# Kernel optimization log

Measured on AMD Instinct MI355X. Metric: run time of the kernel, lower is better.

The kernel has to match this reference:

```python
import jax, jax.numpy as jnp
import numpy as np

S, B, K = 64, 16, 512
QD, KD, A = 512, 512, 256


def setup_inputs() -> dict:
    key = jax.random.key(0)
    ks = jax.random.split(key, 10)
    inv_q = 1.0 / np.sqrt(QD)
    inv_k = 1.0 / np.sqrt(KD)
    inv_a = 1.0 / np.sqrt(A)
    return {
        "queries": jax.random.normal(ks[0], (S, B, QD), dtype=jnp.float32),
        "keys": jax.random.normal(ks[1], (B, K, KD), dtype=jnp.float32),
        "null_mask": jax.random.randint(ks[2], (B, K), 0, 2).astype(jnp.bool_),
        # nn.Linear params (PyTorch layout: weight (out, in), bias (out,))
        "Ww": jax.random.uniform(ks[3], (A, QD), jnp.float32, -inv_q, inv_q),
        "Wb": jax.random.uniform(ks[4], (A,), jnp.float32, -inv_q, inv_q),
        "Uw": jax.random.uniform(ks[5], (A, KD), jnp.float32, -inv_k, inv_k),
        "Ub": jax.random.uniform(ks[6], (A,), jnp.float32, -inv_k, inv_k),
        "vw": jax.random.uniform(ks[7], (1, A), jnp.float32, -inv_a, inv_a),
        "vb": jax.random.uniform(ks[8], (1,), jnp.float32, -inv_a, inv_a),
    }


def reference(queries, keys, null_mask, Ww, Wb, Uw, Ub, vw, vb):
    # t_query: (S, B, A); t_key: (B, K, A)
    t_query = jnp.einsum("sbq,aq->sba", queries, Ww) + Wb
    t_key = jnp.einsum("bkd,ad->bka", keys, Uw) + Ub
    # broadcast add -> (S, B, K, A), tanh, project with v -> alpha (S, B, K)
    h = jnp.tanh(t_query[:, :, None, :] + t_key[None, :, :, :])
    alpha = jnp.einsum("sbka,a->sbk", h, vw[0]) + vb[0]
    alpha = jnp.where(null_mask[None, :, :], -jnp.inf, alpha)
    att_weight = jax.nn.softmax(alpha, axis=2)  # (S, B, K)
    # bmm(att_weight^T, keys)^T -> (S, B, KD)
    attened_keys = jnp.einsum("sbk,bkd->sbd", att_weight, keys)
    return attened_keys, alpha
```

## Files before the change

kernel.cpp:

```cpp
#include <hip/hip_runtime.h>
#include <math.h>

#define S_DIM 64
#define B_DIM 16
#define K_DIM 512
#define QD_DIM 512
#define A_DIM 256

#define NEG_BIG (-3.0e38f)

#define SC 2.8853900817779268f

#define TK_OFF 262144
#define W_WS_OFF ((size_t)2359296)
#define PART_OFF ((size_t)2883584)
#define CONV_F32_OFF ((size_t)4980736)
#define CONV_ROWS 9728
#define LO_USHORT_OFF ((size_t)CONV_ROWS * 512)

typedef __attribute__((ext_vector_type(8))) short short8v;
typedef __attribute__((ext_vector_type(4))) float f32x4;

static __device__ __forceinline__ uint2 pack_hi4(float4 v) {
    unsigned x0 = __float_as_uint(v.x), x1 = __float_as_uint(v.y),
             x2 = __float_as_uint(v.z), x3 = __float_as_uint(v.w);
    uint2 r;
    r.x = (x1 & 0xffff0000u) | (x0 >> 16);
    r.y = (x3 & 0xffff0000u) | (x2 >> 16);
    return r;
}
static __device__ __forceinline__ uint2 pack_lo4(float4 v) {
    float l0 = v.x - __uint_as_float(__float_as_uint(v.x) & 0xffff0000u);
    float l1 = v.y - __uint_as_float(__float_as_uint(v.y) & 0xffff0000u);
    float l2 = v.z - __uint_as_float(__float_as_uint(v.z) & 0xffff0000u);
    float l3 = v.w - __uint_as_float(__float_as_uint(v.w) & 0xffff0000u);
    unsigned y0 = __float_as_uint(l0), y1 = __float_as_uint(l1),
             y2 = __float_as_uint(l2), y3 = __float_as_uint(l3);
    uint2 r;
    r.x = (y1 & 0xffff0000u) | (y0 >> 16);
    r.y = (y3 & 0xffff0000u) | (y2 >> 16);
    return r;
}

__global__ __launch_bounds__(256) void conv_kernel(
    const float* __restrict__ q, const float* __restrict__ k,
    const float* __restrict__ ww, const float* __restrict__ uw,
    unsigned short* __restrict__ hi, unsigned short* __restrict__ lo)
{
    const int idx = blockIdx.x * 256 + threadIdx.x;
    const int row = idx >> 6;
    const int c   = (idx & 63) << 3;

    const float* __restrict__ src;
    if (row < 1024)      src = q  + (size_t)row * 512;
    else if (row < 9216) src = k  + (size_t)(row - 1024) * 512;
    else if (row < 9472) src = ww + (size_t)(row - 9216) * 512;
    else                 src = uw + (size_t)(row - 9472) * 512;

    float4 v0 = *(const float4*)(src + c);
    float4 v1 = *(const float4*)(src + c + 4);
    uint2 h0 = pack_hi4(v0), h1 = pack_hi4(v1);
    uint2 l0 = pack_lo4(v0), l1 = pack_lo4(v1);
    uint4 H = {h0.x, h0.y, h1.x, h1.y};
    uint4 L = {l0.x, l0.y, l1.x, l1.y};
    *(uint4*)&hi[(size_t)row * 512 + c] = H;
    *(uint4*)&lo[(size_t)row * 512 + c] = L;
}

__global__ __launch_bounds__(256) void lin_mfma(
    const unsigned short* __restrict__ hi, const unsigned short* __restrict__ lo,
    const float* __restrict__ Wb, const float* __restrict__ Ub,
    float* __restrict__ t_ws)
{
    __shared__ unsigned short Ah[64][40], Al[64][40], Bh[64][40], Bl[64][40];

    const int bx = blockIdx.x;
    const bool isQ = (bx < 64);
    int mt, nt;
    if (isQ) { mt = bx >> 2; nt = bx & 3; }
    else     { int t = bx - 64; mt = t >> 7; nt = t & 127; }

    const int aro = isQ ? (mt * 64) : (9472 + mt * 64);
    const int bro = isQ ? (9216 + nt * 64) : (1024 + nt * 64);

    const int tid  = threadIdx.x;
    const int srow = tid >> 2;
    const int scol = (tid & 3) << 3;
    const int lane = tid & 63, wid = tid >> 6;
    const int wm = (wid >> 1) << 5, wn = (wid & 1) << 5;
    const int fr  = lane & 15;
    const int fkb = (lane >> 4) << 3;

    f32x4 acc[2][2] = {};

    const unsigned short* pAh = hi + (size_t)(aro + srow) * 512 + scol;
    const unsigned short* pAl = lo + (size_t)(aro + srow) * 512 + scol;
    const unsigned short* pBh = hi + (size_t)(bro + srow) * 512 + scol;
    const unsigned short* pBl = lo + (size_t)(bro + srow) * 512 + scol;

    uint4 c_ah = *(const uint4*)(pAh);
    uint4 c_al = *(const uint4*)(pAl);
    uint4 c_bh = *(const uint4*)(pBh);
    uint4 c_bl = *(const uint4*)(pBl);
    uint4 n_ah = *(const uint4*)(pAh + 32);
    uint4 n_al = *(const uint4*)(pAl + 32);
    uint4 n_bh = *(const uint4*)(pBh + 32);
    uint4 n_bl = *(const uint4*)(pBl + 32);

    for (int ks = 0; ks < 16; ++ks) {
        __syncthreads();
        *(uint4*)&Ah[srow][scol] = c_ah;
        *(uint4*)&Al[srow][scol] = c_al;
        *(uint4*)&Bh[srow][scol] = c_bh;
        *(uint4*)&Bl[srow][scol] = c_bl;
        __syncthreads();
        c_ah = n_ah; c_al = n_al; c_bh = n_bh; c_bl = n_bl;
        if (ks < 14) {
            const int o = (ks + 2) * 32;
            n_ah = *(const uint4*)(pAh + o);
            n_al = *(const uint4*)(pAl + o);
            n_bh = *(const uint4*)(pBh + o);
            n_bl = *(const uint4*)(pBl + o);
        }
        short8v bhv[2], blv[2];
        #pragma unroll
        for (int j = 0; j < 2; ++j) {
            bhv[j] = *(const short8v*)&Bh[wn + j * 16 + fr][fkb];
            blv[j] = *(const short8v*)&Bl[wn + j * 16 + fr][fkb];
        }
        #pragma unroll
        for (int i = 0; i < 2; ++i) {
            short8v ah = *(const short8v*)&Ah[wm + i * 16 + fr][fkb];
            short8v al = *(const short8v*)&Al[wm + i * 16 + fr][fkb];
            #pragma unroll
            for (int j = 0; j < 2; ++j) {
                acc[i][j] = __builtin_amdgcn_mfma_f32_16x16x32_bf16(ah, bhv[j], acc[i][j], 0, 0, 0);
                acc[i][j] = __builtin_amdgcn_mfma_f32_16x16x32_bf16(ah, blv[j], acc[i][j], 0, 0, 0);
                acc[i][j] = __builtin_amdgcn_mfma_f32_16x16x32_bf16(al, bhv[j], acc[i][j], 0, 0, 0);
            }
        }
    }

    const int crow = (lane >> 4) << 2;
    if (isQ) {
        #pragma unroll
        for (int j = 0; j < 2; ++j) {
            const int a_col = nt * 64 + wn + j * 16 + fr;
            const float bias = Wb[a_col];
            #pragma unroll
            for (int i = 0; i < 2; ++i)
                #pragma unroll
                for (int r = 0; r < 4; ++r) {
                    const int m = mt * 64 + wm + i * 16 + crow + r;
                    t_ws[(size_t)m * 256 + a_col] =
                        __builtin_amdgcn_exp2f(SC * (acc[i][j][r] + bias));
                }
        }
    } else {
        #pragma unroll
        for (int i = 0; i < 2; ++i)
            #pragma unroll
            for (int r = 0; r < 4; ++r) {
                const int a = mt * 64 + wm + i * 16 + crow + r;
                const float bias = Ub[a];
                #pragma unroll
                for (int j = 0; j < 2; ++j) {
                    const int n = nt * 64 + wn + j * 16 + fr;
                    t_ws[TK_OFF + (size_t)(n >> 9) * 131072 + (size_t)a * 512 + (n & 511)]
                        = __builtin_amdgcn_exp2f(SC * (acc[i][j][r] + bias));
                }
            }
    }
}

__global__ __launch_bounds__(256) void alpha_part_kernel(
    const float* __restrict__ t_ws, const float* __restrict__ vw,
    float* __restrict__ part)
{
    __shared__ float4 pv[64];

    const int bid = blockIdx.x;
    const int b     = bid >> 7;
    const int inner = bid & 127;
    const int ah    = inner >> 5;
    const int sp    = (inner & 31) << 1;
    const int a0    = ah << 6;
    const int tid = threadIdx.x;

    if (tid < 64) {
        const int a = a0 + tid;
        float4 p;
        p.x = t_ws[(size_t)(sp * B_DIM + b) * A_DIM + a];
        p.y = t_ws[(size_t)((sp + 1) * B_DIM + b) * A_DIM + a];
        p.z = vw[a]; p.w = 0.f;
        pv[tid] = p;
    }
    __syncthreads();

    const float* __restrict__ ek =
        t_ws + TK_OFF + (size_t)b * 131072 + (size_t)a0 * 512;
    const int k2 = tid * 2;

    float acc00 = 0.f, acc01 = 0.f, acc10 = 0.f, acc11 = 0.f;
    #pragma unroll 4
    for (int a = 0; a < 64; ++a) {
        float2 tv = *(const float2*)&ek[(size_t)a * 512 + k2];
        float4 p = pv[a];
        float r00 = __builtin_amdgcn_rcpf(fmaf(p.x, tv.x, 1.0f));
        float r01 = __builtin_amdgcn_rcpf(fmaf(p.x, tv.y, 1.0f));
        float r10 = __builtin_amdgcn_rcpf(fmaf(p.y, tv.x, 1.0f));
        float r11 = __builtin_amdgcn_rcpf(fmaf(p.y, tv.y, 1.0f));
        acc00 = fmaf(p.z, r00, acc00);
        acc01 = fmaf(p.z, r01, acc01);
        acc10 = fmaf(p.z, r10, acc10);
        acc11 = fmaf(p.z, r11, acc11);
    }

    const int sb0 = sp * B_DIM + b;
    float* __restrict__ pp = part + (size_t)ah * 524288;
    *(float2*)&pp[(size_t)sb0 * 512 + k2]           = make_float2(acc00, acc01);
    *(float2*)&pp[(size_t)(sb0 + B_DIM) * 512 + k2] = make_float2(acc10, acc11);
}

__global__ __launch_bounds__(256) void softmax_kernel(
    const float* __restrict__ part, const float* __restrict__ vw,
    const float* __restrict__ vb, const unsigned char* __restrict__ mask,
    float* __restrict__ alpha_out, float* __restrict__ w_ws)
{
    __shared__ float red[3][4];

    const int bid = blockIdx.x;
    const int s = bid >> 4, b = bid & 15;
    const int sb = s * B_DIM + b;
    const int tid = threadIdx.x;
    const int lane = tid & 63, wid = tid >> 6;

    float sv = vw[tid];
    #pragma unroll
    for (int o = 32; o > 0; o >>= 1) sv += __shfl_xor(sv, o);
    if (lane == 0) red[0][wid] = sv;
    __syncthreads();
    const float base = red[0][0] + red[0][1] + red[0][2] + red[0][3] + vb[0];

    const int k2 = tid * 2;
    const size_t po = (size_t)sb * 512 + k2;
    float2 p0 = *(const float2*)&part[po];
    float2 p1 = *(const float2*)&part[po + 524288];
    float2 p2 = *(const float2*)&part[po + 2 * 524288];
    float2 p3 = *(const float2*)&part[po + 3 * 524288];
    float a0 = base - 2.0f * (p0.x + p1.x + p2.x + p3.x);
    float a1 = base - 2.0f * (p0.y + p1.y + p2.y + p3.y);

    const unsigned char* mrow = mask + b * K_DIM;
    if (mrow[k2])     a0 = NEG_BIG;
    if (mrow[k2 + 1]) a1 = NEG_BIG;

    *(float2*)&alpha_out[(size_t)sb * K_DIM + k2] = make_float2(a0, a1);

    float m = fmaxf(a0, a1);
    #pragma unroll
    for (int o = 32; o > 0; o >>= 1) m = fmaxf(m, __shfl_xor(m, o));
    if (lane == 0) red[1][wid] = m;
    __syncthreads();
    const float mx = fmaxf(fmaxf(red[1][0], red[1][1]), fmaxf(red[1][2], red[1][3]));

    float e0 = __expf(a0 - mx);
    float e1 = __expf(a1 - mx);
    float ssum = e0 + e1;
    #pragma unroll
    for (int o = 32; o > 0; o >>= 1) ssum += __shfl_xor(ssum, o);
    if (lane == 0) red[2][wid] = ssum;
    __syncthreads();
    const float inv = 1.0f / (red[2][0] + red[2][1] + red[2][2] + red[2][3]);

    *(float2*)&w_ws[(size_t)(b * S_DIM + s) * K_DIM + k2] = make_float2(e0 * inv, e1 * inv);
}

__global__ __launch_bounds__(256) void att_kernel(
    const float* __restrict__ w_ws, const float* __restrict__ keys,
    float* __restrict__ out_att)
{
    __shared__ float wt[16][68];
    __shared__ float kt[64][64];

    const int d0g = blockIdx.x * 64;
    const int s0  = blockIdx.y * 16;
    const int b   = blockIdx.z;
    const int tid = threadIdx.x;

    const int sL = tid >> 4;
    const int dc = (tid & 15) << 2;

    float acc[4] = {};

    for (int k0 = 0; k0 < K_DIM; k0 += 64) {
        __syncthreads();
        *(float4*)&wt[sL][dc] =
            *(const float4*)&w_ws[(size_t)(b * S_DIM + s0 + sL) * K_DIM + k0 + dc];
        #pragma unroll
        for (int rr = 0; rr < 4; ++rr) {
            const int kr = (tid >> 4) + rr * 16;
            *(float4*)&kt[kr][dc] =
                *(const float4*)&keys[((size_t)b * K_DIM + k0 + kr) * QD_DIM + d0g + dc];
        }
        __syncthreads();
        #pragma unroll
        for (int kk = 0; kk < 64; kk += 4) {
            float4 wv = *(const float4*)&wt[sL][kk];
            float wr[4] = {wv.x, wv.y, wv.z, wv.w};
            #pragma unroll
            for (int u = 0; u < 4; ++u) {
                float4 kv = *(const float4*)&kt[kk + u][dc];
                acc[0] = fmaf(wr[u], kv.x, acc[0]);
                acc[1] = fmaf(wr[u], kv.y, acc[1]);
                acc[2] = fmaf(wr[u], kv.z, acc[2]);
                acc[3] = fmaf(wr[u], kv.w, acc[3]);
            }
        }
    }

    float4 o = {acc[0], acc[1], acc[2], acc[3]};
    *(float4*)&out_att[(size_t)((s0 + sL) * B_DIM + b) * QD_DIM + d0g + dc] = o;
}

extern "C" void kernel_launch(void* const* d_in, const int* in_sizes, int n_in,
                              void* d_out, int out_size, void* d_ws, size_t ws_size,
                              hipStream_t stream) {
    const float* queries = (const float*)d_in[0];
    const float* keys    = (const float*)d_in[1];
    const unsigned char* mask = (const unsigned char*)d_in[2];
    const float* Ww = (const float*)d_in[3];
    const float* Wb = (const float*)d_in[4];
    const float* Uw = (const float*)d_in[5];
    const float* Ub = (const float*)d_in[6];
    const float* vw = (const float*)d_in[7];
    const float* vb = (const float*)d_in[8];

    float* out_att   = (float*)d_out;
    float* out_alpha = (float*)d_out + (size_t)S_DIM * B_DIM * QD_DIM;

    float* t_ws = (float*)d_ws;
    float* w_ws = t_ws + W_WS_OFF;
    float* part = t_ws + PART_OFF;
    unsigned short* hi = (unsigned short*)(t_ws + CONV_F32_OFF);
    unsigned short* lo = hi + LO_USHORT_OFF;

    conv_kernel<<<2432, 256, 0, stream>>>(queries, keys, Ww, Uw, hi, lo);

    lin_mfma<<<576, 256, 0, stream>>>(hi, lo, Wb, Ub, t_ws);

    alpha_part_kernel<<<2048, 256, 0, stream>>>(t_ws, vw, part);

    softmax_kernel<<<1024, 256, 0, stream>>>(part, vw, vb, mask,
                                             out_alpha, w_ws);

    dim3 gC(QD_DIM / 64, S_DIM / 16, B_DIM);
    att_kernel<<<gC, 256, 0, stream>>>(w_ws, keys, out_att);
}
```

Before: 143.4 us.

## Fuse alpha partial-sum kernel into softmax kernel, dropping partials buffer

Merges the alpha partial-sum kernel (split over four A chunks and two s rows per block) with the softmax kernel, so each block computes the full 256-wide A reduction for one (s,b) row and then does masking and softmax in place. This removes one launch and the write and read of a 2M-float partials buffer. In exchange each block now loops over all of A serially with only one s row per block, losing the reuse of t_key loads across two s rows and reducing parallelism per output element. Block order is remapped so that pairs of b alternate, which appears aimed at L2 locality of t_key across blocks.

```diff
diff --git a/kernel.cpp b/kernel.cpp
--- a/kernel.cpp
+++ b/kernel.cpp
@@ -13,8 +13,7 @@
 
 #define TK_OFF 262144
 #define W_WS_OFF ((size_t)2359296)
-#define PART_OFF ((size_t)2883584)
-#define CONV_F32_OFF ((size_t)4980736)
+#define CONV_F32_OFF ((size_t)2883584)
 #define CONV_ROWS 9728
 #define LO_USHORT_OFF ((size_t)CONV_ROWS * 512)
 
@@ -173,84 +172,54 @@
     }
 }
 
-__global__ __launch_bounds__(256) void alpha_part_kernel(
+__global__ __launch_bounds__(256) void alpha_kernel(
     const float* __restrict__ t_ws, const float* __restrict__ vw,
-    float* __restrict__ part)
-{
-    __shared__ float4 pv[64];
-
-    const int bid = blockIdx.x;
-    const int b     = bid >> 7;
-    const int inner = bid & 127;
-    const int ah    = inner >> 5;
-    const int sp    = (inner & 31) << 1;
-    const int a0    = ah << 6;
-    const int tid = threadIdx.x;
-
-    if (tid < 64) {
-        const int a = a0 + tid;
-        float4 p;
-        p.x = t_ws[(size_t)(sp * B_DIM + b) * A_DIM + a];
-        p.y = t_ws[(size_t)((sp + 1) * B_DIM + b) * A_DIM + a];
-        p.z = vw[a]; p.w = 0.f;
-        pv[tid] = p;
-    }
-    __syncthreads();
-
-    const float* __restrict__ ek =
-        t_ws + TK_OFF + (size_t)b * 131072 + (size_t)a0 * 512;
-    const int k2 = tid * 2;
-
-    float acc00 = 0.f, acc01 = 0.f, acc10 = 0.f, acc11 = 0.f;
-    #pragma unroll 4
-    for (int a = 0; a < 64; ++a) {
-        float2 tv = *(const float2*)&ek[(size_t)a * 512 + k2];
-        float4 p = pv[a];
-        float r00 = __builtin_amdgcn_rcpf(fmaf(p.x, tv.x, 1.0f));
-        float r01 = __builtin_amdgcn_rcpf(fmaf(p.x, tv.y, 1.0f));
-        float r10 = __builtin_amdgcn_rcpf(fmaf(p.y, tv.x, 1.0f));
-        float r11 = __builtin_amdgcn_rcpf(fmaf(p.y, tv.y, 1.0f));
-        acc00 = fmaf(p.z, r00, acc00);
-        acc01 = fmaf(p.z, r01, acc01);
-        acc10 = fmaf(p.z, r10, acc10);
-        acc11 = fmaf(p.z, r11, acc11);
-    }
-
-    const int sb0 = sp * B_DIM + b;
-    float* __restrict__ pp = part + (size_t)ah * 524288;
-    *(float2*)&pp[(size_t)sb0 * 512 + k2]           = make_float2(acc00, acc01);
-    *(float2*)&pp[(size_t)(sb0 + B_DIM) * 512 + k2] = make_float2(acc10, acc11);
-}
-
-__global__ __launch_bounds__(256) void softmax_kernel(
-    const float* __restrict__ part, const float* __restrict__ vw,
     const float* __restrict__ vb, const unsigned char* __restrict__ mask,
     float* __restrict__ alpha_out, float* __restrict__ w_ws)
 {
+    __shared__ float2 pv[256];
     __shared__ float red[3][4];
 
     const int bid = blockIdx.x;
-    const int s = bid >> 4, b = bid & 15;
+    const int x = bid & 7;
+    const int j = bid >> 3;
+    const int b = (x << 1) | (j & 1);
+    const int s = j >> 1;
     const int sb = s * B_DIM + b;
     const int tid = threadIdx.x;
     const int lane = tid & 63, wid = tid >> 6;
 
-    float sv = vw[tid];
+    const float myvw = vw[tid];
+    {
+        float2 p;
+        p.x = t_ws[(size_t)sb * A_DIM + tid];
+        p.y = myvw;
+        pv[tid] = p;
+    }
+
+    float sv = myvw;
     #pragma unroll
     for (int o = 32; o > 0; o >>= 1) sv += __shfl_xor(sv, o);
     if (lane == 0) red[0][wid] = sv;
     __syncthreads();
     const float base = red[0][0] + red[0][1] + red[0][2] + red[0][3] + vb[0];
 
+    const float* __restrict__ ek = t_ws + TK_OFF + (size_t)b * 131072;
     const int k2 = tid * 2;
-    const size_t po = (size_t)sb * 512 + k2;
-    float2 p0 = *(const float2*)&part[po];
-    float2 p1 = *(const float2*)&part[po + 524288];
-    float2 p2 = *(const float2*)&part[po + 2 * 524288];
-    float2 p3 = *(const float2*)&part[po + 3 * 524288];
-    float a0 = base - 2.0f * (p0.x + p1.x + p2.x + p3.x);
-    float a1 = base - 2.0f * (p0.y + p1.y + p2.y + p3.y);
-
+
+    float acc0 = 0.f, acc1 = 0.f;
+    #pragma unroll 8
+    for (int a = 0; a < A_DIM; ++a) {
+        float2 tv = *(const float2*)&ek[(size_t)a * 512 + k2];
+        float2 p = pv[a];
+        float r0 = __builtin_amdgcn_rcpf(fmaf(p.x, tv.x, 1.0f));
+        float r1 = __builtin_amdgcn_rcpf(fmaf(p.x, tv.y, 1.0f));
+        acc0 = fmaf(p.y, r0, acc0);
+        acc1 = fmaf(p.y, r1, acc1);
+    }
+
+    float a0 = base - 2.0f * acc0;
+    float a1 = base - 2.0f * acc1;
     const unsigned char* mrow = mask + b * K_DIM;
     if (mrow[k2])     a0 = NEG_BIG;
     if (mrow[k2 + 1]) a1 = NEG_BIG;
@@ -341,7 +310,6 @@
 
     float* t_ws = (float*)d_ws;
     float* w_ws = t_ws + W_WS_OFF;
-    float* part = t_ws + PART_OFF;
     unsigned short* hi = (unsigned short*)(t_ws + CONV_F32_OFF);
     unsigned short* lo = hi + LO_USHORT_OFF;
 
@@ -349,10 +317,8 @@
 
     lin_mfma<<<576, 256, 0, stream>>>(hi, lo, Wb, Ub, t_ws);
 
-    alpha_part_kernel<<<2048, 256, 0, stream>>>(t_ws, vw, part);
-
-    softmax_kernel<<<1024, 256, 0, stream>>>(part, vw, vb, mask,
-                                             out_alpha, w_ws);
+    alpha_kernel<<<1024, 256, 0, stream>>>(t_ws, vw, vb, mask,
+                                           out_alpha, w_ws);
 
     dim3 gC(QD_DIM / 64, S_DIM / 16, B_DIM);
     att_kernel<<<gC, 256, 0, stream>>>(w_ws, keys, out_att);
```

Result: slower. 148.9 us (+3.8%).
